# Kernel optimization log

Hardware: AMD Instinct MI355X
Metric: run time of the kernel (lower is better)

The kernel has to match this reference:

```python
import jax, jax.numpy as jnp
import numpy as np

N, E, G = 20480, 163840, 512          # nodes, edges, graphs
D, H, R, L = 128, 4, 8, 4             # embed dim, heads, relations, layers
HK = H * D                            # heads * out_channels (RGATConv internal width)
BOARD_WIDTH = 7
NEG_SLOPE = 0.2                       # RGATConv leaky_relu slope


def setup_inputs() -> dict:
    key = jax.random.key(0)
    ks = jax.random.split(key, 12)
    s_in = 1.0 / np.sqrt(D)
    s_att = 1.0 / np.sqrt(HK)
    return {
        "x_nodes": jax.random.randint(ks[0], (N,), 0, 3),
        "edge_index": jax.random.randint(ks[1], (2, E), 0, N),
        "edge_type": jax.random.randint(ks[2], (E,), 0, R),
        "batch": jnp.arange(N) // (N // G),  # G graphs of N//G nodes each
        "emb": jax.random.normal(ks[3], (3, D), jnp.float32),
        "W": jax.random.normal(ks[4], (L, R, D, HK), jnp.float32) * s_in,
        "Q": jax.random.normal(ks[5], (L, HK, H), jnp.float32) * s_att,
        "K": jax.random.normal(ks[6], (L, HK, H), jnp.float32) * s_att,
        "B": jnp.zeros((L, D), jnp.float32),
        "fc1_w": jax.random.normal(ks[7], (D, 64), jnp.float32) * s_in,
        "fc1_b": jnp.zeros((64,), jnp.float32),
        "pol_w": jax.random.normal(ks[8], (64, BOARD_WIDTH), jnp.float32) * 0.125,
        "pol_b": jnp.zeros((BOARD_WIDTH,), jnp.float32),
        "val_w": jax.random.normal(ks[9], (64, 1), jnp.float32) * 0.125,
        "val_b": jnp.zeros((1,), jnp.float32),
    }


def _rgat_layer(x, W, Q, Km, b, src, dst, etype):
    # RGATConv, additive-self-attention, across-relation softmax, concat=False.
    x_all = jnp.einsum('nd,rdk->nrk', x, W)          # [N,R,HK] per-relation transform
    q_all = jnp.einsum('nrk,kh->nrh', x_all, Q)      # [N,R,H]
    k_all = jnp.einsum('nrk,kh->nrh', x_all, Km)     # [N,R,H]
    alpha = jax.nn.leaky_relu(q_all[dst, etype] + k_all[src, etype], NEG_SLOPE)  # [E,H]
    # segment softmax over destination nodes (across all relations)
    amax = jax.lax.stop_gradient(jax.ops.segment_max(alpha, dst, num_segments=N))
    ex = jnp.exp(alpha - amax[dst])
    denom = jax.ops.segment_sum(ex, dst, num_segments=N)
    a = ex / (denom[dst] + 1e-16)                    # [E,H]
    msg = x_all[src, etype].reshape(E, H, D) * a[:, :, None]   # [E,H,D]
    agg = jax.ops.segment_sum(msg.reshape(E, HK), dst, num_segments=N)
    out = agg.reshape(N, H, D).mean(axis=1) + b      # head-mean (concat=False) + bias
    return jax.nn.relu(out)


def reference(x_nodes, edge_index, edge_type, batch, emb, W, Q, K, B,
              fc1_w, fc1_b, pol_w, pol_b, val_w, val_b):
    src, dst = edge_index[0], edge_index[1]
    x = emb[x_nodes]                                  # [N,D]
    for l in range(L):
        x = _rgat_layer(x, W[l], Q[l], K[l], B[l], src, dst, edge_type)
    cnt = jax.ops.segment_sum(jnp.ones((N,), x.dtype), batch, num_segments=G)
    pooled = jax.ops.segment_sum(x, batch, num_segments=G) / jnp.maximum(cnt, 1.0)[:, None]
    h = jax.nn.relu(pooled @ fc1_w + fc1_b)           # [G,64]
    policy = h @ pol_w + pol_b                        # [G,BOARD_WIDTH]
    value = jnp.tanh(h @ val_w + val_b)               # [G,1]
    return policy, value
```

## Files before the change

kernel.cpp:

```cpp
#include <hip/hip_runtime.h>
#include <cstdint>
#include <cstddef>

constexpr int N_  = 20480;
constexpr int E_  = 163840;
constexpr int G_  = 512;
constexpr int D_  = 128;
constexpr int H_  = 4;
constexpr int R_  = 8;
constexpr int L_  = 4;
constexpr int HK_ = 512;
constexpr int NPG_ = N_ / G_;

typedef short short8 __attribute__((ext_vector_type(8)));
typedef float f32x4 __attribute__((ext_vector_type(4)));
typedef unsigned short u16;
typedef unsigned int u32;

__device__ inline u16 bfr(float f) {
  u32 u = __builtin_bit_cast(u32, f);
  return (u16)((u + 0x7fffu + ((u >> 16) & 1u)) >> 16);
}
__device__ inline float bf2f(u32 lo16) { return __builtin_bit_cast(float, lo16 << 16); }
__device__ inline float lrelu(float v) { return v >= 0.f ? v : 0.2f * v; }

__global__ void k_zero_i(int* __restrict__ p, int n) {
  int i = blockIdx.x * blockDim.x + threadIdx.x;
  if (i < n) p[i] = 0;
}

__global__ void k_count_rel(const int* __restrict__ dst, const int* __restrict__ et,
                            int* __restrict__ counts) {
  int e = blockIdx.x * blockDim.x + threadIdx.x;
  if (e < E_) atomicAdd(&counts[et[e] * N_ + dst[e]], 1);
}
__global__ void k_count_dst(const int* __restrict__ dst, int* __restrict__ counts) {
  int e = blockIdx.x * blockDim.x + threadIdx.x;
  if (e < E_) atomicAdd(&counts[dst[e]], 1);
}
__global__ void k_bsum(const int* __restrict__ c, int* __restrict__ bsum) {
  int t = threadIdx.x;
  const int4 v = *(const int4*)&c[blockIdx.x * 1024 + t * 4];
  int s = v.x + v.y + v.z + v.w;
#pragma unroll
  for (int o = 32; o; o >>= 1) s += __shfl_down(s, o, 64);
  __shared__ int ws_[4];
  if ((t & 63) == 0) ws_[t >> 6] = s;
  __syncthreads();
  if (t == 0) bsum[blockIdx.x] = ws_[0] + ws_[1] + ws_[2] + ws_[3];
}
__global__ void k_bscan(int* __restrict__ bsum, int nb, int* __restrict__ tot_out) {
  __shared__ int sh[512];
  int t = threadIdx.x;
  if (t < nb) sh[t] = bsum[t];
  __syncthreads();
  if (t == 0) {
    int run = 0;
    for (int i = 0; i < nb; ++i) { int v = sh[i]; sh[i] = run; run += v; }
    tot_out[0] = run;
  }
  __syncthreads();
  if (t < nb) bsum[t] = sh[t];
}
__global__ void k_scan3(const int* __restrict__ c, const int* __restrict__ bsum,
                        int* __restrict__ indptr, int* __restrict__ cursor) {
  __shared__ int ts[256];
  int t = threadIdx.x;
  int base = blockIdx.x * 1024 + t * 4;
  const int4 v = *(const int4*)&c[base];
  int s0 = v.x, s01 = v.x + v.y, s012 = s01 + v.z, s = s012 + v.w;
  ts[t] = s;
  __syncthreads();
#pragma unroll
  for (int o = 1; o < 256; o <<= 1) {
    int add = (t >= o) ? ts[t - o] : 0;
    __syncthreads();
    ts[t] += add;
    __syncthreads();
  }
  int off = bsum[blockIdx.x] + (t ? ts[t - 1] : 0);
  int4 o4 = make_int4(off, off + s0, off + s01, off + s012);
  *(int4*)&indptr[base] = o4;
  *(int4*)&cursor[base] = o4;
}
__global__ void k_scatter_rel(const int* __restrict__ dst, const int* __restrict__ et,
                              const int* __restrict__ src, int* __restrict__ cursor,
                              int* __restrict__ esort, int* __restrict__ slotOf,
                              int* __restrict__ srcR) {
  int e = blockIdx.x * blockDim.x + threadIdx.x;
  if (e < E_) {
    int p = atomicAdd(&cursor[et[e] * N_ + dst[e]], 1);
    esort[p] = e;
    slotOf[e] = p;
    srcR[p] = src[e];
  }
}
__global__ void k_scatter_dst(const int* __restrict__ dst, int* __restrict__ cursor,
                              int* __restrict__ esort) {
  int e = blockIdx.x * blockDim.x + threadIdx.x;
  if (e < E_) {
    int p = atomicAdd(&cursor[dst[e]], 1);
    esort[p] = e;
  }
}
__global__ void k_padbase(const int* __restrict__ indptrR, int* __restrict__ padBase) {
  if (threadIdx.x == 0 && blockIdx.x == 0) {
    int cum = 0;
    for (int r = 0; r < R_; ++r) {
      padBase[r] = cum;
      int cnt = indptrR[(r + 1) * N_] - indptrR[r * N_];
      cum += (cnt + 63) & ~63;
    }
    padBase[R_] = cum;
  }
}

__global__ void k_embed(const int* __restrict__ xn, const float* __restrict__ emb,
                        float* __restrict__ x, u16* __restrict__ xb) {
  int i = blockIdx.x * blockDim.x + threadIdx.x;
  if (i < N_ * D_) {
    int n = i >> 7, d = i & 127;
    float v = emb[xn[n] * D_ + d];
    x[i] = v;
    xb[i] = bfr(v);
  }
}

__global__ __launch_bounds__(256) void k_wqk_all(const float* __restrict__ W,
                                                 const float* __restrict__ Q,
                                                 const float* __restrict__ Km,
                                                 float* __restrict__ WQK) {
  int gw = (blockIdx.x * 256 + threadIdx.x) >> 6;
  int lane = threadIdx.x & 63;
  int d = gw & 127, r = (gw >> 7) & 7, l = gw >> 10;
  const float* wrow = W + (((size_t)l * R_ + r) * D_ + d) * HK_;
  const float* Ql = Q + (size_t)l * HK_ * H_;
  const float* Kl = Km + (size_t)l * HK_ * H_;
  float acc[8] = {0.f, 0.f, 0.f, 0.f, 0.f, 0.f, 0.f, 0.f};
#pragma unroll
  for (int it = 0; it < 8; ++it) {
    int k = it * 64 + lane;
    float w = wrow[k];
    const float4 qv = *(const float4*)&Ql[k * 4];
    const float4 kv = *(const float4*)&Kl[k * 4];
    acc[0] += w * qv.x; acc[1] += w * qv.y; acc[2] += w * qv.z; acc[3] += w * qv.w;
    acc[4] += w * kv.x; acc[5] += w * kv.y; acc[6] += w * kv.z; acc[7] += w * kv.w;
  }
#pragma unroll
  for (int o = 32; o; o >>= 1)
#pragma unroll
    for (int j = 0; j < 8; ++j) acc[j] += __shfl_down(acc[j], o, 64);
  if (lane == 0) {
#pragma unroll
    for (int h = 0; h < 4; ++h) {
      WQK[((size_t)l * D_ + d) * 64 + r * 4 + h] = acc[h];
      WQK[((size_t)l * D_ + d) * 64 + 32 + r * 4 + h] = acc[4 + h];
    }
  }
}

__global__ __launch_bounds__(256) void k_qk(const float* __restrict__ x,
                                            const float* __restrict__ WQK,
                                            float* __restrict__ q,
                                            float* __restrict__ kk) {
  __shared__ float xs[32][129];
  __shared__ float wq[128][64];
  const int t = threadIdx.x;
  const int n0 = blockIdx.x * 32;
#pragma unroll
  for (int p = 0; p < 4; ++p) {
    int idx = t + p * 256;
    int row = idx >> 5, c4 = (idx & 31) * 4;
    const float4 v = *(const float4*)&x[(size_t)(n0 + row) * D_ + c4];
    xs[row][c4 + 0] = v.x; xs[row][c4 + 1] = v.y;
    xs[row][c4 + 2] = v.z; xs[row][c4 + 3] = v.w;
  }
#pragma unroll
  for (int p = 0; p < 8; ++p) {
    int idx = t + p * 256;
    int row = idx >> 4, c4 = (idx & 15) * 4;
    *(float4*)&wq[row][c4] = *(const float4*)&WQK[row * 64 + c4];
  }
  __syncthreads();
  const int node = t >> 3, cq = t & 7;
  float s[8];
#pragma unroll
  for (int j = 0; j < 8; ++j) s[j] = 0.f;
  for (int k = 0; k < 128; ++k) {
    float xv = xs[node][k];
#pragma unroll
    for (int j = 0; j < 8; ++j) s[j] = fmaf(xv, wq[k][cq * 8 + j], s[j]);
  }
#pragma unroll
  for (int j = 0; j < 8; ++j) {
    int c = cq * 8 + j;
    if (c < 32) q[(size_t)(n0 + node) * 32 + c] = s[j];
    else        kk[(size_t)(n0 + node) * 32 + (c - 32)] = s[j];
  }
}

__global__ __launch_bounds__(256) void k_attn(
    const int* __restrict__ ipN, const int* __restrict__ esD,
    const int* __restrict__ src, const int* __restrict__ et,
    const float* __restrict__ q, const float* __restrict__ kk,
    const int* __restrict__ slotOf, float* __restrict__ aw) {
  int n = blockIdx.x * 4 + (threadIdx.x >> 6);
  int lane = threadIdx.x & 63;
  int j0 = ipN[n], j1 = ipN[n + 1];
  int deg = j1 - j0;
  if (deg == 0) return;
  int h = lane & 3;
  int nch = (deg + 15) >> 4;
  float m = -3.4e38f;
  for (int c = 0; c < nch; ++c) {
    int ei = c * 16 + (lane >> 2);
    if (ei < deg) {
      int e = esD[j0 + ei];
      int r = et[e];
      float a = lrelu(q[(size_t)n * 32 + r * 4 + h] + kk[(size_t)src[e] * 32 + r * 4 + h]);
      m = fmaxf(m, a);
    }
  }
#pragma unroll
  for (int o = 4; o < 64; o <<= 1) m = fmaxf(m, __shfl_xor(m, o, 64));
  float s = 0.f;
  for (int c = 0; c < nch; ++c) {
    int ei = c * 16 + (lane >> 2);
    if (ei < deg) {
      int e = esD[j0 + ei];
      int r = et[e];
      float a = lrelu(q[(size_t)n * 32 + r * 4 + h] + kk[(size_t)src[e] * 32 + r * 4 + h]);
      float ex = expf(a - m);
      s += ex;
      aw[(size_t)slotOf[e] * 4 + h] = ex;
    }
  }
#pragma unroll
  for (int o = 4; o < 64; o <<= 1) s += __shfl_xor(s, o, 64);
  float inv = 0.25f / (s + 1e-16f);
  for (int c = 0; c < nch; ++c) {
    int ei = c * 16 + (lane >> 2);
    if (ei < deg) {
      int e = esD[j0 + ei];
      aw[(size_t)slotOf[e] * 4 + h] *= inv;
    }
  }
}

__global__ void k_cvt_w_all(const float* __restrict__ W, u16* __restrict__ wt) {
  __shared__ u16 tile[64][65];
  const int z = blockIdx.z, k0 = blockIdx.y * 64, c0 = blockIdx.x * 64;
  const int t = threadIdx.x;
  const int tk = t >> 4, tc4 = (t & 15) * 4;
  const float* Wz = W + (size_t)z * D_ * HK_;
  u16* wz = wt + (size_t)z * HK_ * D_;
#pragma unroll
  for (int p = 0; p < 4; ++p) {
    int krow = tk + p * 16;
    const float4 v = *(const float4*)&Wz[(size_t)(k0 + krow) * HK_ + c0 + tc4];
    tile[tc4 + 0][krow] = bfr(v.x);
    tile[tc4 + 1][krow] = bfr(v.y);
    tile[tc4 + 2][krow] = bfr(v.z);
    tile[tc4 + 3][krow] = bfr(v.w);
  }
  __syncthreads();
#pragma unroll
  for (int p = 0; p < 4; ++p) {
    int crow = tk + p * 16;
    uint2 o;
    o.x = (u32)tile[crow][tc4 + 0] | ((u32)tile[crow][tc4 + 1] << 16);
    o.y = (u32)tile[crow][tc4 + 2] | ((u32)tile[crow][tc4 + 3] << 16);
    *(uint2*)&wz[(size_t)(c0 + crow) * D_ + k0 + tc4] = o;
  }
}

__global__ __launch_bounds__(512) void k_edge5(
    const u16* __restrict__ xb, const u16* __restrict__ wt,
    const int* __restrict__ indptrR, const int* __restrict__ padBase,
    const int* __restrict__ srcR, const float* __restrict__ aw,
    u16* __restrict__ m) {
  __shared__ u16 atile[64 * 128];
  __shared__ float awl[64][4];
  __shared__ int srcl[64];
  const int t = threadIdx.x;
  const int b64 = blockIdx.x * 64;
  if (b64 >= padBase[R_]) return;
  int r = 0;
  while (b64 >= padBase[r + 1]) ++r;
  const int ip0 = indptrR[r * N_];
  const int cnt = indptrR[(r + 1) * N_] - ip0;
  const int local0 = b64 - padBase[r];
  const u16* wrp = wt + (size_t)r * HK_ * D_;
  const int wid = t >> 6, lane = t & 63;
  const int l15 = lane & 15, l4 = lane >> 4;
  short8 breg[4][4];
#pragma unroll
  for (int ks = 0; ks < 4; ++ks)
#pragma unroll
    for (int h = 0; h < 4; ++h) {
      int c = (wid + 8 * h) * 16 + l15;
      breg[ks][h] = *(const short8*)(wrp + (size_t)c * 128 + ks * 32 + l4 * 8);
    }
  if (t < 64) {
    int lidx = local0 + t;
    if (lidx < cnt) {
      srcl[t] = srcR[ip0 + lidx];
      *(float4*)awl[t] = *(const float4*)(aw + (size_t)(ip0 + lidx) * 4);
    } else {
      srcl[t] = 0;
      *(float4*)awl[t] = make_float4(0.f, 0.f, 0.f, 0.f);
    }
  }
  __syncthreads();
#pragma unroll
  for (int p = 0; p < 2; ++p) {
    int idx = t + p * 512;
    int row = idx >> 4, seg = idx & 15;
    uint4 v = *(const uint4*)(xb + (size_t)srcl[row] * 128 + seg * 8);
    *(uint4*)((char*)atile + row * 256 + ((seg * 16) ^ ((row & 7) << 4))) = v;
  }
  __syncthreads();
  f32x4 acc[4][4];
#pragma unroll
  for (int i = 0; i < 4; ++i)
#pragma unroll
    for (int h = 0; h < 4; ++h) acc[i][h] = (f32x4){0.f, 0.f, 0.f, 0.f};
#pragma unroll
  for (int ks = 0; ks < 4; ++ks) {
    short8 av[4];
#pragma unroll
    for (int i = 0; i < 4; ++i) {
      int row = i * 16 + l15;
      av[i] = *(const short8*)((char*)atile + row * 256 +
                ((l4 * 16 + ks * 64) ^ ((row & 7) << 4)));
    }
#pragma unroll
    for (int i = 0; i < 4; ++i)
#pragma unroll
      for (int h = 0; h < 4; ++h)
        acc[i][h] = __builtin_amdgcn_mfma_f32_16x16x32_bf16(breg[ks][h], av[i],
                                                            acc[i][h], 0, 0, 0);
  }
#pragma unroll
  for (int i = 0; i < 4; ++i) {
    int row = i * 16 + l15;
    const float4 awf = *(const float4*)awl[row];
    float v0 = awf.x * acc[i][0][0] + awf.y * acc[i][1][0] + awf.z * acc[i][2][0] + awf.w * acc[i][3][0];
    float v1 = awf.x * acc[i][0][1] + awf.y * acc[i][1][1] + awf.z * acc[i][2][1] + awf.w * acc[i][3][1];
    float v2 = awf.x * acc[i][0][2] + awf.y * acc[i][1][2] + awf.z * acc[i][2][2] + awf.w * acc[i][3][2];
    float v3 = awf.x * acc[i][0][3] + awf.y * acc[i][1][3] + awf.z * acc[i][2][3] + awf.w * acc[i][3][3];
    uint2 o;
    o.x = (u32)bfr(v0) | ((u32)bfr(v1) << 16);
    o.y = (u32)bfr(v2) | ((u32)bfr(v3) << 16);
    *(uint2*)(m + (size_t)(b64 + row) * 128 + wid * 16 + l4 * 4) = o;
  }
}

__global__ __launch_bounds__(256) void k_agg2(
    const int* __restrict__ indptrR, const int* __restrict__ padBase,
    const u16* __restrict__ m, const float* __restrict__ Bl,
    float* __restrict__ xout, u16* __restrict__ xbout) {
  int n = blockIdx.x * 4 + (threadIdx.x >> 6);
  int lane = threadIdx.x & 63;
  float s0 = 0.f, s1 = 0.f;
#pragma unroll
  for (int r = 0; r < R_; ++r) {
    int ip0 = indptrR[r * N_];
    int j0 = indptrR[r * N_ + n], j1 = indptrR[r * N_ + n + 1];
    int base = padBase[r] + (j0 - ip0);
    for (int j = 0; j < j1 - j0; ++j) {
      u32 v = *((const u32*)(m + (size_t)(base + j) * 128) + lane);
      s0 += bf2f(v & 0xffffu);
      s1 += bf2f(v >> 16);
    }
  }
  float2 o;
  o.x = fmaxf(s0 + Bl[2 * lane], 0.f);
  o.y = fmaxf(s1 + Bl[2 * lane + 1], 0.f);
  *((float2*)(xout + (size_t)n * D_) + lane) = o;
  ((u32*)(xbout + (size_t)n * D_))[lane] = (u32)bfr(o.x) | ((u32)bfr(o.y) << 16);
}

__global__ void k_pool(const float* __restrict__ x, float* __restrict__ pooled) {
  int i = blockIdx.x * blockDim.x + threadIdx.x;
  if (i >= G_ * D_) return;
  int d = i & 127, g = i >> 7;
  float s = 0.f;
  for (int j = 0; j < NPG_; ++j) s += x[(size_t)(g * NPG_ + j) * D_ + d];
  pooled[i] = s * (1.0f / NPG_);
}

__global__ void k_head(const float* __restrict__ pooled, const float* __restrict__ fc1w,
                       const float* __restrict__ fc1b, const float* __restrict__ polw,
                       const float* __restrict__ polb, const float* __restrict__ valw,
                       const float* __restrict__ valb, float* __restrict__ out) {
  int g = blockIdx.x;
  int t = threadIdx.x;
  __shared__ float hb[64];
  const float* p = pooled + (size_t)g * D_;
  float s = fc1b[t];
  for (int d = 0; d < D_; ++d) s += p[d] * fc1w[d * 64 + t];
  hb[t] = fmaxf(s, 0.f);
  __syncthreads();
  if (t < 7) {
    float s2 = polb[t];
    for (int j = 0; j < 64; ++j) s2 += hb[j] * polw[j * 7 + t];
    out[g * 7 + t] = s2;
  } else if (t == 7) {
    float s2 = valb[0];
    for (int j = 0; j < 64; ++j) s2 += hb[j] * valw[j];
    out[G_ * 7 + g] = tanhf(s2);
  }
}

extern "C" void kernel_launch(void* const* d_in, const int* in_sizes, int n_in,
                              void* d_out, int out_size, void* d_ws, size_t ws_size,
                              hipStream_t stream) {
  (void)in_sizes; (void)n_in; (void)out_size;
  const int*   x_nodes = (const int*)d_in[0];
  const int*   eidx    = (const int*)d_in[1];
  const int*   etype   = (const int*)d_in[2];
  const float* emb     = (const float*)d_in[4];
  const float* W       = (const float*)d_in[5];
  const float* Q       = (const float*)d_in[6];
  const float* Km      = (const float*)d_in[7];
  const float* B       = (const float*)d_in[8];
  const float* fc1w    = (const float*)d_in[9];
  const float* fc1b    = (const float*)d_in[10];
  const float* polw    = (const float*)d_in[11];
  const float* polb    = (const float*)d_in[12];
  const float* valw    = (const float*)d_in[13];
  const float* valb    = (const float*)d_in[14];
  float* out = (float*)d_out;
  const int* srcA = eidx;
  const int* dstA = eidx + E_;

  char* p = (char*)d_ws;
  size_t used = 0;
  auto carve = [&](size_t bytes) {
    char* q = p;
    size_t adv = (bytes + 255) & ~(size_t)255;
    p += adv;
    used += adv;
    return q;
  };
  float* x_cur  = (float*)carve((size_t)N_ * D_ * 4);
  float* x_nxt  = (float*)carve((size_t)N_ * D_ * 4);
  u16*   xbf    = (u16*)carve((size_t)N_ * D_ * 2);
  u16*   mbuf   = (u16*)carve((size_t)(E_ + 512) * D_ * 2);
  float* qbuf   = (float*)carve((size_t)N_ * 32 * 4);
  float* kbuf   = (float*)carve((size_t)N_ * 32 * 4);
  float* awbuf  = (float*)carve((size_t)E_ * H_ * 4);
  float* WQKb   = (float*)carve((size_t)L_ * D_ * 64 * 4);
  u16*   Wtb    = (u16*)carve((size_t)L_ * R_ * HK_ * D_ * 2);
  float* pooled = (float*)carve((size_t)G_ * D_ * 4);
  int* countsR  = (int*)carve((size_t)R_ * N_ * 4);
  int* cursorR  = (int*)carve((size_t)R_ * N_ * 4);
  int* indptrR  = (int*)carve((size_t)(R_ * N_ + 1) * 4);
  int* esortR   = (int*)carve((size_t)E_ * 4);
  int* slotOf   = (int*)carve((size_t)E_ * 4);
  int* srcR     = (int*)carve((size_t)E_ * 4);
  int* countsN  = (int*)carve((size_t)N_ * 4);
  int* cursorN  = (int*)carve((size_t)N_ * 4);
  int* indptrN  = (int*)carve((size_t)(N_ + 1) * 4);
  int* esortD   = (int*)carve((size_t)E_ * 4);
  int* padBase  = (int*)carve((size_t)(R_ + 1) * 4);
  int* bsum     = (int*)carve((size_t)512 * 4);
  if (used > ws_size) return;

  constexpr int RN = R_ * N_;
  constexpr int NBR = RN / 1024;
  constexpr int NBN = N_ / 1024;
  constexpr int EDGE_BLOCKS = E_ / 64 + R_;

  k_zero_i<<<(RN + 255) / 256, 256, 0, stream>>>(countsR, RN);
  k_zero_i<<<(N_ + 255) / 256, 256, 0, stream>>>(countsN, N_);
  k_count_rel<<<E_ / 256, 256, 0, stream>>>(dstA, etype, countsR);
  k_count_dst<<<E_ / 256, 256, 0, stream>>>(dstA, countsN);
  k_bsum<<<NBR, 256, 0, stream>>>(countsR, bsum);
  k_bscan<<<1, 512, 0, stream>>>(bsum, NBR, indptrR + RN);
  k_scan3<<<NBR, 256, 0, stream>>>(countsR, bsum, indptrR, cursorR);
  k_scatter_rel<<<E_ / 256, 256, 0, stream>>>(dstA, etype, srcA, cursorR, esortR,
                                              slotOf, srcR);
  k_bsum<<<NBN, 256, 0, stream>>>(countsN, bsum);
  k_bscan<<<1, 512, 0, stream>>>(bsum, NBN, indptrN + N_);
  k_scan3<<<NBN, 256, 0, stream>>>(countsN, bsum, indptrN, cursorN);
  k_scatter_dst<<<E_ / 256, 256, 0, stream>>>(dstA, cursorN, esortD);
  k_padbase<<<1, 64, 0, stream>>>(indptrR, padBase);
  k_embed<<<(N_ * D_) / 256, 256, 0, stream>>>(x_nodes, emb, x_cur, xbf);
  k_wqk_all<<<(L_ * R_ * D_ * 64) / 256, 256, 0, stream>>>(W, Q, Km, WQKb);
  k_cvt_w_all<<<dim3(HK_ / 64, D_ / 64, L_ * R_), 256, 0, stream>>>(W, Wtb);

  for (int l = 0; l < L_; ++l) {
    const float* Bl = B + (size_t)l * D_;
    k_qk<<<N_ / 32, 256, 0, stream>>>(x_cur, WQKb + (size_t)l * D_ * 64, qbuf, kbuf);
    k_attn<<<N_ / 4, 256, 0, stream>>>(indptrN, esortD, srcA, etype, qbuf, kbuf,
                                       slotOf, awbuf);
    k_edge5<<<EDGE_BLOCKS, 512, 0, stream>>>(xbf, Wtb + (size_t)l * R_ * HK_ * D_,
                                             indptrR, padBase, srcR, awbuf, mbuf);
    k_agg2<<<N_ / 4, 256, 0, stream>>>(indptrR, padBase, mbuf, Bl, x_nxt, xbf);
    float* tmp = x_cur; x_cur = x_nxt; x_nxt = tmp;
  }

  k_pool<<<(G_ * D_) / 256, 256, 0, stream>>>(x_cur, pooled);
  k_head<<<G_, 64, 0, stream>>>(pooled, fc1w, fc1b, polw, polb, valw, valb, out);
}
```

Before: 544.1 us.

## Fuse next-layer q/k projection into aggregation, enlarge edge GEMM tiles, fast-path small-degree attention

Several changes land together. The aggregation kernel now also computes the next layer's q/k projections from the freshly produced node row, using the projection matrix staged in shared memory, so the separate per-layer k_qk launch and its re-read of x go away. The edge GEMM kernel now handles 128 edges per block with a single-block occupancy hint, and stages its bf16 output through LDS so global stores are coalesced. Attention gains a single-pass path for nodes with at most 16 incoming edges, and aggregation unrolls its loop by two. The costs are 32KB of shared memory and an extra sync in the aggregation kernel, plus lower occupancy and more padding in the edge kernel.

```diff
diff --git a/kernel.cpp b/kernel.cpp
--- a/kernel.cpp
+++ b/kernel.cpp
@@ -109,7 +109,7 @@
     for (int r = 0; r < R_; ++r) {
       padBase[r] = cum;
       int cnt = indptrR[(r + 1) * N_] - indptrR[r * N_];
-      cum += (cnt + 63) & ~63;
+      cum += (cnt + 127) & ~127;
     }
     padBase[R_] = cum;
   }
@@ -210,6 +210,26 @@
   int deg = j1 - j0;
   if (deg == 0) return;
   int h = lane & 3;
+  if (deg <= 16) {
+    int ei = lane >> 2;
+    float a = -3.4e38f;
+    int slot = 0;
+    if (ei < deg) {
+      int e = esD[j0 + ei];
+      int r = et[e];
+      slot = slotOf[e];
+      a = lrelu(q[(size_t)n * 32 + r * 4 + h] + kk[(size_t)src[e] * 32 + r * 4 + h]);
+    }
+    float m = a;
+#pragma unroll
+    for (int o = 4; o < 64; o <<= 1) m = fmaxf(m, __shfl_xor(m, o, 64));
+    float ex = (ei < deg) ? expf(a - m) : 0.f;
+    float s = ex;
+#pragma unroll
+    for (int o = 4; o < 64; o <<= 1) s += __shfl_xor(s, o, 64);
+    if (ei < deg) aw[(size_t)slot * 4 + h] = ex * (0.25f / (s + 1e-16f));
+    return;
+  }
   int nch = (deg + 15) >> 4;
   float m = -3.4e38f;
   for (int c = 0; c < nch; ++c) {
@@ -274,22 +294,22 @@
   }
 }
 
-__global__ __launch_bounds__(512) void k_edge5(
+__global__ __launch_bounds__(512, 1) void k_edge7(
     const u16* __restrict__ xb, const u16* __restrict__ wt,
     const int* __restrict__ indptrR, const int* __restrict__ padBase,
     const int* __restrict__ srcR, const float* __restrict__ aw,
     u16* __restrict__ m) {
-  __shared__ u16 atile[64 * 128];
-  __shared__ float awl[64][4];
-  __shared__ int srcl[64];
+  __shared__ u16 atile[128 * 128];
+  __shared__ float awl[128][4];
+  __shared__ int srcl[128];
   const int t = threadIdx.x;
-  const int b64 = blockIdx.x * 64;
-  if (b64 >= padBase[R_]) return;
+  const int b128 = blockIdx.x * 128;
+  if (b128 >= padBase[R_]) return;
   int r = 0;
-  while (b64 >= padBase[r + 1]) ++r;
+  while (b128 >= padBase[r + 1]) ++r;
   const int ip0 = indptrR[r * N_];
   const int cnt = indptrR[(r + 1) * N_] - ip0;
-  const int local0 = b64 - padBase[r];
+  const int local0 = b128 - padBase[r];
   const u16* wrp = wt + (size_t)r * HK_ * D_;
   const int wid = t >> 6, lane = t & 63;
   const int l15 = lane & 15, l4 = lane >> 4;
@@ -301,7 +321,7 @@
       int c = (wid + 8 * h) * 16 + l15;
       breg[ks][h] = *(const short8*)(wrp + (size_t)c * 128 + ks * 32 + l4 * 8);
     }
-  if (t < 64) {
+  if (t < 128) {
     int lidx = local0 + t;
     if (lidx < cnt) {
       srcl[t] = srcR[ip0 + lidx];
@@ -313,36 +333,37 @@
   }
   __syncthreads();
 #pragma unroll
-  for (int p = 0; p < 2; ++p) {
+  for (int p = 0; p < 4; ++p) {
     int idx = t + p * 512;
     int row = idx >> 4, seg = idx & 15;
     uint4 v = *(const uint4*)(xb + (size_t)srcl[row] * 128 + seg * 8);
     *(uint4*)((char*)atile + row * 256 + ((seg * 16) ^ ((row & 7) << 4))) = v;
   }
   __syncthreads();
-  f32x4 acc[4][4];
-#pragma unroll
-  for (int i = 0; i < 4; ++i)
+  f32x4 acc[8][4];
+#pragma unroll
+  for (int i = 0; i < 8; ++i)
 #pragma unroll
     for (int h = 0; h < 4; ++h) acc[i][h] = (f32x4){0.f, 0.f, 0.f, 0.f};
 #pragma unroll
   for (int ks = 0; ks < 4; ++ks) {
-    short8 av[4];
-#pragma unroll
-    for (int i = 0; i < 4; ++i) {
+    short8 av[8];
+#pragma unroll
+    for (int i = 0; i < 8; ++i) {
       int row = i * 16 + l15;
       av[i] = *(const short8*)((char*)atile + row * 256 +
                 ((l4 * 16 + ks * 64) ^ ((row & 7) << 4)));
     }
 #pragma unroll
-    for (int i = 0; i < 4; ++i)
+    for (int i = 0; i < 8; ++i)
 #pragma unroll
       for (int h = 0; h < 4; ++h)
         acc[i][h] = __builtin_amdgcn_mfma_f32_16x16x32_bf16(breg[ks][h], av[i],
                                                             acc[i][h], 0, 0, 0);
   }
-#pragma unroll
-  for (int i = 0; i < 4; ++i) {
+  __syncthreads();
+#pragma unroll
+  for (int i = 0; i < 8; ++i) {
     int row = i * 16 + l15;
     const float4 awf = *(const float4*)awl[row];
     float v0 = awf.x * acc[i][0][0] + awf.y * acc[i][1][0] + awf.z * acc[i][2][0] + awf.w * acc[i][3][0];
@@ -352,26 +373,55 @@
     uint2 o;
     o.x = (u32)bfr(v0) | ((u32)bfr(v1) << 16);
     o.y = (u32)bfr(v2) | ((u32)bfr(v3) << 16);
-    *(uint2*)(m + (size_t)(b64 + row) * 128 + wid * 16 + l4 * 4) = o;
-  }
-}
-
-__global__ __launch_bounds__(256) void k_agg2(
+    *(uint2*)((char*)atile + row * 256 + ((wid * 32 + l4 * 8) ^ ((row & 7) << 4))) = o;
+  }
+  __syncthreads();
+  {
+    int row = t >> 2, c0 = (t & 3) * 64;
+    char* gout = (char*)(m + (size_t)(b128 + row) * 128) + c0;
+#pragma unroll
+    for (int qq = 0; qq < 4; ++qq) {
+      uint4 v = *(const uint4*)((char*)atile + row * 256 + ((c0 + qq * 16) ^ ((row & 7) << 4)));
+      *(uint4*)(gout + qq * 16) = v;
+    }
+  }
+}
+
+__global__ __launch_bounds__(256) void k_aggqk(
     const int* __restrict__ indptrR, const int* __restrict__ padBase,
     const u16* __restrict__ m, const float* __restrict__ Bl,
-    float* __restrict__ xout, u16* __restrict__ xbout) {
-  int n = blockIdx.x * 4 + (threadIdx.x >> 6);
-  int lane = threadIdx.x & 63;
+    const float* __restrict__ WQK, int doqk,
+    float* __restrict__ xout, u16* __restrict__ xbout,
+    float* __restrict__ q, float* __restrict__ kk) {
+  __shared__ float wqs[128 * 64];
+  __shared__ float xrow[4][128];
+  const int t = threadIdx.x;
+  if (doqk) {
+#pragma unroll
+    for (int p = 0; p < 8; ++p)
+      *(float4*)&wqs[(t + p * 256) * 4] = *(const float4*)&WQK[(t + p * 256) * 4];
+  }
+  const int w = t >> 6;
+  int n = blockIdx.x * 4 + w;
+  int lane = t & 63;
   float s0 = 0.f, s1 = 0.f;
 #pragma unroll
   for (int r = 0; r < R_; ++r) {
     int ip0 = indptrR[r * N_];
     int j0 = indptrR[r * N_ + n], j1 = indptrR[r * N_ + n + 1];
     int base = padBase[r] + (j0 - ip0);
-    for (int j = 0; j < j1 - j0; ++j) {
-      u32 v = *((const u32*)(m + (size_t)(base + j) * 128) + lane);
-      s0 += bf2f(v & 0xffffu);
-      s1 += bf2f(v >> 16);
+    int cntn = j1 - j0;
+    int j = 0;
+    for (; j + 1 < cntn; j += 2) {
+      u32 v0 = *((const u32*)(m + (size_t)(base + j) * 128) + lane);
+      u32 v1 = *((const u32*)(m + (size_t)(base + j + 1) * 128) + lane);
+      s0 += bf2f(v0 & 0xffffu) + bf2f(v1 & 0xffffu);
+      s1 += bf2f(v0 >> 16) + bf2f(v1 >> 16);
+    }
+    if (j < cntn) {
+      u32 v0 = *((const u32*)(m + (size_t)(base + j) * 128) + lane);
+      s0 += bf2f(v0 & 0xffffu);
+      s1 += bf2f(v0 >> 16);
     }
   }
   float2 o;
@@ -379,6 +429,21 @@
   o.y = fmaxf(s1 + Bl[2 * lane + 1], 0.f);
   *((float2*)(xout + (size_t)n * D_) + lane) = o;
   ((u32*)(xbout + (size_t)n * D_))[lane] = (u32)bfr(o.x) | ((u32)bfr(o.y) << 16);
+  if (doqk) {
+    xrow[w][2 * lane] = o.x;
+    xrow[w][2 * lane + 1] = o.y;
+    __syncthreads();
+    const float* xr = xrow[w];
+    float s = 0.f;
+#pragma unroll
+    for (int d4 = 0; d4 < 32; ++d4) {
+      const float4 xv = *(const float4*)&xr[d4 * 4];
+      s += xv.x * wqs[(d4 * 4 + 0) * 64 + lane] + xv.y * wqs[(d4 * 4 + 1) * 64 + lane] +
+           xv.z * wqs[(d4 * 4 + 2) * 64 + lane] + xv.w * wqs[(d4 * 4 + 3) * 64 + lane];
+    }
+    if (lane < 32) q[(size_t)n * 32 + lane] = s;
+    else           kk[(size_t)n * 32 + (lane - 32)] = s;
+  }
 }
 
 __global__ void k_pool(const float* __restrict__ x, float* __restrict__ pooled) {
@@ -447,7 +512,7 @@
   float* x_cur  = (float*)carve((size_t)N_ * D_ * 4);
   float* x_nxt  = (float*)carve((size_t)N_ * D_ * 4);
   u16*   xbf    = (u16*)carve((size_t)N_ * D_ * 2);
-  u16*   mbuf   = (u16*)carve((size_t)(E_ + 512) * D_ * 2);
+  u16*   mbuf   = (u16*)carve((size_t)(E_ + R_ * 128) * D_ * 2);
   float* qbuf   = (float*)carve((size_t)N_ * 32 * 4);
   float* kbuf   = (float*)carve((size_t)N_ * 32 * 4);
   float* awbuf  = (float*)carve((size_t)E_ * H_ * 4);
@@ -471,7 +536,7 @@
   constexpr int RN = R_ * N_;
   constexpr int NBR = RN / 1024;
   constexpr int NBN = N_ / 1024;
-  constexpr int EDGE_BLOCKS = E_ / 64 + R_;
+  constexpr int EDGE_BLOCKS = E_ / 128 + R_;
 
   k_zero_i<<<(RN + 255) / 256, 256, 0, stream>>>(countsR, RN);
   k_zero_i<<<(N_ + 255) / 256, 256, 0, stream>>>(countsN, N_);
@@ -490,15 +555,18 @@
   k_embed<<<(N_ * D_) / 256, 256, 0, stream>>>(x_nodes, emb, x_cur, xbf);
   k_wqk_all<<<(L_ * R_ * D_ * 64) / 256, 256, 0, stream>>>(W, Q, Km, WQKb);
   k_cvt_w_all<<<dim3(HK_ / 64, D_ / 64, L_ * R_), 256, 0, stream>>>(W, Wtb);
+  k_qk<<<N_ / 32, 256, 0, stream>>>(x_cur, WQKb, qbuf, kbuf);
 
   for (int l = 0; l < L_; ++l) {
     const float* Bl = B + (size_t)l * D_;
-    k_qk<<<N_ / 32, 256, 0, stream>>>(x_cur, WQKb + (size_t)l * D_ * 64, qbuf, kbuf);
     k_attn<<<N_ / 4, 256, 0, stream>>>(indptrN, esortD, srcA, etype, qbuf, kbuf,
                                        slotOf, awbuf);
-    k_edge5<<<EDGE_BLOCKS, 512, 0, stream>>>(xbf, Wtb + (size_t)l * R_ * HK_ * D_,
+    k_edge7<<<EDGE_BLOCKS, 512, 0, stream>>>(xbf, Wtb + (size_t)l * R_ * HK_ * D_,
                                              indptrR, padBase, srcR, awbuf, mbuf);
-    k_agg2<<<N_ / 4, 256, 0, stream>>>(indptrR, padBase, mbuf, Bl, x_nxt, xbf);
+    int doqk = (l < L_ - 1) ? 1 : 0;
+    k_aggqk<<<N_ / 4, 256, 0, stream>>>(indptrR, padBase, mbuf, Bl,
+                                        WQKb + (size_t)(l + 1) * D_ * 64 * (doqk ? 1 : 0),
+                                        doqk, x_nxt, xbf, qbuf, kbuf);
     float* tmp = x_cur; x_cur = x_nxt; x_nxt = tmp;
   }
 
```

Result: faster. 532.7 us (-2.1%).
